# Optimization experiments

Measured on AMD Instinct MI355X. Metric: run time of the kernel, lower is better.

## Reference

```python
import jax, jax.numpy as jnp
import numpy as np

# Problem sizes (batched graph of G molecules)
N = 100_000   # total nodes
E = 400_000   # total directed edges
G = 2_500     # number of molecule graphs
K = 3         # len(idx_wo_smiles) -> zero rows inserted
NODE_F = 74   # graph_feats_shape[0]
EDGE_F = 12   # graph_feats_shape[1]
HID = 128     # hidden_feats = dim // 2
DIM = 256     # dim


def setup_inputs() -> dict:
    key = jax.random.key(0)
    ks = jax.random.split(key, 20)
    init = lambda k, shape, fan: (jax.random.normal(k, shape, jnp.float32) / np.sqrt(fan)).astype(jnp.float32)

    node_feats = jax.random.normal(ks[0], (N, NODE_F), jnp.float32)
    edge_feats = jax.random.normal(ks[1], (E, EDGE_F), jnp.float32)  # passed but unused by GCN
    src = jax.random.randint(ks[2], (E,), 0, N)
    dst = jax.random.randint(ks[3], (E,), 0, N)
    # sorted graph ids, every graph non-empty (~40 atoms each)
    graph_ids = (jnp.arange(N) * G) // N
    idx_wo_smiles = jnp.arange(K)

    return {
        'node_feats': node_feats,
        'edge_feats': edge_feats,
        'W1': init(ks[4], (NODE_F, HID), NODE_F), 'b1': jnp.zeros((HID,), jnp.float32),
        'Wr1': init(ks[5], (NODE_F, HID), NODE_F), 'br1': jnp.zeros((HID,), jnp.float32),
        'W2': init(ks[6], (HID, HID), HID), 'b2': jnp.zeros((HID,), jnp.float32),
        'Wr2': init(ks[7], (HID, HID), HID), 'br2': jnp.zeros((HID,), jnp.float32),
        'w_atom': init(ks[8], (HID, 1), HID), 'b_atom': jnp.zeros((1,), jnp.float32),
        'Wp1': init(ks[9], (2 * HID, HID), 2 * HID), 'bp1': jnp.zeros((HID,), jnp.float32),
        'Wp2': init(ks[10], (HID, DIM), HID), 'bp2': jnp.zeros((DIM,), jnp.float32),
        'src': src, 'dst': dst, 'graph_ids': graph_ids, 'idx_wo_smiles': idx_wo_smiles,
    }


def reference(node_feats, edge_feats, W1, b1, Wr1, br1, W2, b2, Wr2, br2,
              w_atom, b_atom, Wp1, bp1, Wp2, bp2, src, dst, graph_ids, idx_wo_smiles):
    n = node_feats.shape[0]
    ones_e = jnp.ones(src.shape[0], jnp.float32)
    out_deg = jax.ops.segment_sum(ones_e, src, num_segments=n)
    in_deg = jax.ops.segment_sum(ones_e, dst, num_segments=n)
    norm_s = jax.lax.rsqrt(jnp.maximum(out_deg, 1.0))  # [N]
    norm_d = jax.lax.rsqrt(jnp.maximum(in_deg, 1.0))   # [N]

    def gcn_layer(h, W, b, Wr, br):
        # GraphConv(norm='both'): D^-1/2 A D^-1/2 h W + b, with relu activation
        m = h[src] * norm_s[src][:, None]                       # [E, F] gather
        agg = jax.ops.segment_sum(m, dst, num_segments=n)       # [N, F] scatter-add
        gc = jax.nn.relu((agg * norm_d[:, None]) @ W + b)
        res = jax.nn.relu(h @ Wr + br)                          # residual connection
        return gc + res

    h = gcn_layer(node_feats, W1, b1, Wr1, br1)   # [N, HID]
    h = gcn_layer(h, W2, b2, Wr2, br2)            # [N, HID]

    # WeightedSumAndMax readout per molecule
    aw = jax.nn.sigmoid(h @ w_atom + b_atom)                          # [N, 1]
    hsum = jax.ops.segment_sum(h * aw, graph_ids, num_segments=G)     # [G, HID]
    hmax = jax.ops.segment_max(h, graph_ids, num_segments=G)          # [G, HID]
    gfeat = jnp.concatenate([hsum, hmax], axis=1)                     # [G, 2*HID]

    latent = jax.nn.relu(gfeat @ Wp1 + bp1) @ Wp2 + bp2               # [G, DIM]

    # Insert zero rows at idx_wo_smiles (sorted ascending -> final positions)
    total = G + idx_wo_smiles.shape[0]
    zero_mask = jnp.zeros((total,), bool).at[idx_wo_smiles].set(True)
    keep = jnp.nonzero(~zero_mask, size=G)[0]
    out = jnp.zeros((total, latent.shape[1]), latent.dtype).at[keep].set(latent)
    return out
```

## Files before the change

kernel.cpp:

```cpp
#include <hip/hip_runtime.h>
#include <hip/hip_bf16.h>
#include <stdint.h>

#define NODE_F 74
#define HID 128
#define DIM 256

typedef __hip_bfloat16 bf16;
typedef unsigned int u32;
typedef unsigned short u16;

typedef short s16x8 __attribute__((ext_vector_type(8)));
typedef __bf16 bf16x8 __attribute__((ext_vector_type(8)));
typedef float f32x4 __attribute__((ext_vector_type(4)));

__device__ __forceinline__ float rdl(float v, int l){
  return __int_as_float(__builtin_amdgcn_readlane(__float_as_int(v), l));
}
__device__ __forceinline__ float2 bfpair(u32 u){
  float2 r;
  r.x = __uint_as_float(u << 16);
  r.y = __uint_as_float(u & 0xffff0000u);
  return r;
}
__device__ __forceinline__ u32 packbf(float a, float b){
  u32 lo = (u32)__bfloat16_as_ushort(__float2bfloat16(a));
  u32 hi = (u32)__bfloat16_as_ushort(__float2bfloat16(b));
  return lo | (hi << 16);
}
__device__ __forceinline__ u16 bfbits(float a){
  return __bfloat16_as_ushort(__float2bfloat16(a));
}

__global__ void k_deg_prep(const int* __restrict__ src, const int* __restrict__ dst_,
                           float* __restrict__ outdeg_f, int* __restrict__ indeg, int E_,
                           const float* __restrict__ W1, const float* __restrict__ Wr1,
                           const float* __restrict__ W2, const float* __restrict__ Wr2,
                           u16* __restrict__ Bp1, u16* __restrict__ Bp2){
  int e = blockIdx.x*256 + threadIdx.x;
  if (e < E_){
    atomicAdd(&outdeg_f[src[e]], 1.0f);
    atomicAdd(&indeg[dst_[e]], 1);
  }
  int idx = e;
  if (idx < 57344){
    const float* W; u16* dstp; int S, Ktrue, loc;
    if      (idx < 12288){ W = W1;  dstp = Bp1;          S = 3; Ktrue = NODE_F; loc = idx; }
    else if (idx < 24576){ W = Wr1; dstp = Bp1 + 12288;  S = 3; Ktrue = NODE_F; loc = idx - 12288; }
    else if (idx < 40960){ W = W2;  dstp = Bp2;          S = 4; Ktrue = HID;    loc = idx - 24576; }
    else                 { W = Wr2; dstp = Bp2 + 16384;  S = 4; Ktrue = HID;    loc = idx - 40960; }
    const int el  = loc & 7;
    const int l   = (loc >> 3) & 63;
    const int rem = loc >> 9;
    const int s   = rem % S;
    const int t   = rem / S;
    const int k   = s*32 + (l >> 4)*8 + el;
    const int c   = t*16 + (l & 15);
    const float v = (k < Ktrue) ? W[(size_t)k*HID + c] : 0.f;
    dstp[loc] = bfbits(v);
  }
}

__global__ __launch_bounds__(256) void k_scan_a(const int* __restrict__ indeg,
                                                float* __restrict__ norm_s,
                                                float* __restrict__ norm_d,
                                                int* __restrict__ bsum, int n){
  __shared__ int red[256];
  const int base = blockIdx.x*1024 + threadIdx.x*4;
  int s = 0;
  #pragma unroll
  for (int i = 0; i < 4; ++i){
    const int idx = base + i;
    if (idx < n){
      const int d = indeg[idx];
      s += d;
      norm_d[idx] = rsqrtf(fmaxf((float)d, 1.0f));
      norm_s[idx] = rsqrtf(fmaxf(norm_s[idx], 1.0f));
    }
  }
  red[threadIdx.x] = s;
  __syncthreads();
  #pragma unroll
  for (int off = 128; off; off >>= 1){
    if (threadIdx.x < off) red[threadIdx.x] += red[threadIdx.x + off];
    __syncthreads();
  }
  if (threadIdx.x == 0) bsum[blockIdx.x] = red[0];
}

__global__ __launch_bounds__(1024) void k_scan_b(int* __restrict__ bsum, int nb){
  __shared__ int part[1024];
  __shared__ int carry;
  if (threadIdx.x == 0) carry = 0;
  __syncthreads();
  for (int c0 = 0; c0 < nb; c0 += 1024){
    const int tid = threadIdx.x, idx = c0 + tid;
    part[tid] = (idx < nb) ? bsum[idx] : 0;
    __syncthreads();
    for (int off = 1; off < 1024; off <<= 1){
      const int t = (tid >= off) ? part[tid-off] : 0;
      __syncthreads();
      part[tid] += t;
      __syncthreads();
    }
    if (idx < nb) bsum[idx] = carry + ((tid == 0) ? 0 : part[tid-1]);
    __syncthreads();
    if (tid == 0) carry += part[1023];
    __syncthreads();
  }
}

__global__ __launch_bounds__(256) void k_scan_c(int* __restrict__ indeg,
                                                const int* __restrict__ bsum,
                                                int* __restrict__ row_ptr, int n){
  __shared__ int part[256];
  const int base = blockIdx.x*1024 + threadIdx.x*4;
  int v[4]; int s = 0;
  #pragma unroll
  for (int i = 0; i < 4; ++i){
    const int idx = base + i;
    v[i] = (idx < n) ? indeg[idx] : 0;
    s += v[i];
  }
  part[threadIdx.x] = s;
  __syncthreads();
  for (int off = 1; off < 256; off <<= 1){
    const int t = (threadIdx.x >= off) ? part[threadIdx.x-off] : 0;
    __syncthreads();
    part[threadIdx.x] += t;
    __syncthreads();
  }
  int run = bsum[blockIdx.x] + ((threadIdx.x == 0) ? 0 : part[threadIdx.x-1]);
  #pragma unroll
  for (int i = 0; i < 4; ++i){
    const int idx = base + i;
    if (idx < n){
      row_ptr[idx] = run;
      run += v[i];
      indeg[idx] = 0;
    }
    if (idx == n-1) row_ptr[n] = run;
  }
}

__global__ void k_fill_conv(const int* __restrict__ src, const int* __restrict__ dst,
                            const int* __restrict__ row_ptr, int* __restrict__ cursor,
                            int* __restrict__ col, int E_,
                            const float* __restrict__ x0,
                            const float* __restrict__ norm_s,
                            u32* __restrict__ x0bf, int n, int do_conv){
  int e = blockIdx.x*256 + threadIdx.x;
  if (e < E_){
    int d = dst[e];
    int pos = row_ptr[d] + atomicAdd(&cursor[d], 1);
    col[pos] = src[e];
  }
  if (do_conv){
    const int tot = n*48;
    if (e < tot){
      const int r = e/48, l = e - r*48;
      const int f0 = 2*l, f1 = 2*l + 1;
      const float ns = norm_s[r];
      const float u0 = (f0 < NODE_F) ? ns*x0[(size_t)r*NODE_F + f0] : 0.f;
      const float u1 = (f1 < NODE_F) ? ns*x0[(size_t)r*NODE_F + f1] : 0.f;
      x0bf[e] = packbf(u0, u1);
    }
  }
}

__global__ __launch_bounds__(256, 8) void k_gather1b(
    const u32* __restrict__ x0bf, const int* __restrict__ row_ptr,
    const int* __restrict__ col, const float* __restrict__ norm_d,
    u32* __restrict__ ag1, int n){
  const int lane = threadIdx.x & 63;
  const int wv   = (blockIdx.x*256 + threadIdx.x) >> 6;
  const int r0   = wv*2;
  if (r0 >= n) return;
  int p[2], e[2];
  p[0] = row_ptr[r0]; e[0] = row_ptr[r0+1];
  const bool ok1 = (r0+1) < n;
  p[1] = ok1 ? e[0] : 0;
  e[1] = ok1 ? row_ptr[r0+2] : 0;
  const bool act = (lane < 48);
  const u32* xb = x0bf + lane;
  float a0[2] = {0.f,0.f}, a1[2] = {0.f,0.f};
  while ((p[0] < e[0]) | (p[1] < e[1])){
    int c[2], s[2][4];
    #pragma unroll
    for (int i = 0; i < 2; ++i){
      int d = e[i] - p[i];
      c[i] = (d > 4) ? 4 : ((d < 0) ? 0 : d);
      if (c[i] > 0){
        #pragma unroll
        for (int j = 0; j < 4; ++j)
          s[i][j] = col[p[i] + ((j < c[i]) ? j : (c[i]-1))];
      }
    }
    u32 v[2][4];
    #pragma unroll
    for (int i = 0; i < 2; ++i){
      #pragma unroll
      for (int j = 0; j < 4; ++j) v[i][j] = 0u;
      if (c[i] > 0 && act){
        #pragma unroll
        for (int j = 0; j < 4; ++j){
          const u32 t = xb[(size_t)s[i][j]*48];
          v[i][j] = (j < c[i]) ? t : 0u;
        }
      }
    }
    #pragma unroll
    for (int i = 0; i < 2; ++i){
      const float2 f0 = bfpair(v[i][0]), f1 = bfpair(v[i][1]);
      const float2 f2 = bfpair(v[i][2]), f3 = bfpair(v[i][3]);
      a0[i] += (f0.x + f1.x) + (f2.x + f3.x);
      a1[i] += (f0.y + f1.y) + (f2.y + f3.y);
      p[i] += c[i];
    }
  }
  if (lane < 48){
    #pragma unroll
    for (int i = 0; i < 2; ++i){
      const int row = r0 + i;
      if (row < n){
        const float nd = norm_d[row];
        ag1[(size_t)row*48 + lane] = packbf(a0[i]*nd, a1[i]*nd);
      }
    }
  }
}

__global__ __launch_bounds__(256, 8) void k_gather2b(
    const u32* __restrict__ h1u, const int* __restrict__ row_ptr,
    const int* __restrict__ col, const float* __restrict__ norm_s,
    const float* __restrict__ norm_d, u32* __restrict__ ag2, int n){
  const int lane = threadIdx.x & 63;
  const int wv   = (blockIdx.x*256 + threadIdx.x) >> 6;
  const int r0   = wv*2;
  if (r0 >= n) return;
  int p[2], e[2];
  p[0] = row_ptr[r0]; e[0] = row_ptr[r0+1];
  const bool ok1 = (r0+1) < n;
  p[1] = ok1 ? e[0] : 0;
  e[1] = ok1 ? row_ptr[r0+2] : 0;
  const u32* hb = h1u + lane;
  float a0[2] = {0.f,0.f}, a1[2] = {0.f,0.f};
  while ((p[0] < e[0]) | (p[1] < e[1])){
    int c[2], s[2][4];
    #pragma unroll
    for (int i = 0; i < 2; ++i){
      int d = e[i] - p[i];
      c[i] = (d > 4) ? 4 : ((d < 0) ? 0 : d);
      if (c[i] > 0){
        #pragma unroll
        for (int j = 0; j < 4; ++j)
          s[i][j] = col[p[i] + ((j < c[i]) ? j : (c[i]-1))];
      }
    }
    float nw[2][4];
    u32 v[2][4];
    #pragma unroll
    for (int i = 0; i < 2; ++i){
      #pragma unroll
      for (int j = 0; j < 4; ++j){ nw[i][j] = 0.f; v[i][j] = 0u; }
      if (c[i] > 0){
        #pragma unroll
        for (int j = 0; j < 4; ++j) nw[i][j] = (j < c[i]) ? norm_s[s[i][j]] : 0.f;
        #pragma unroll
        for (int j = 0; j < 4; ++j) v[i][j] = hb[(size_t)s[i][j]*64];
      }
    }
    #pragma unroll
    for (int i = 0; i < 2; ++i){
      const float2 f0 = bfpair(v[i][0]), f1 = bfpair(v[i][1]);
      const float2 f2 = bfpair(v[i][2]), f3 = bfpair(v[i][3]);
      a0[i] = fmaf(f0.x, nw[i][0], fmaf(f1.x, nw[i][1],
              fmaf(f2.x, nw[i][2], fmaf(f3.x, nw[i][3], a0[i]))));
      a1[i] = fmaf(f0.y, nw[i][0], fmaf(f1.y, nw[i][1],
              fmaf(f2.y, nw[i][2], fmaf(f3.y, nw[i][3], a1[i]))));
      p[i] += c[i];
    }
  }
  #pragma unroll
  for (int i = 0; i < 2; ++i){
    const int row = r0 + i;
    if (row < n){
      const float nd = norm_d[row];
      ag2[(size_t)row*64 + lane] = packbf(a0[i]*nd, a1[i]*nd);
    }
  }
}

__global__ __launch_bounds__(256) void k_gather1f(
    const float* __restrict__ x0, const int* __restrict__ row_ptr,
    const int* __restrict__ col, const float* __restrict__ norm_s,
    const float* __restrict__ norm_d, u32* __restrict__ ag1, int n){
  const int lane = threadIdx.x & 63;
  const int row  = blockIdx.x*4 + (threadIdx.x >> 6);
  if (row >= n) return;
  const int p0 = row_ptr[row], p1 = row_ptr[row+1];
  const bool act = (lane < 37);
  const float* xb = x0 + 2*lane;
  float a0 = 0.f, a1 = 0.f;
  int p = p0;
  #pragma unroll 1
  for (; p + 3 < p1; p += 4){
    const int s0 = col[p], s1 = col[p+1], s2 = col[p+2], s3 = col[p+3];
    const float n0 = norm_s[s0], n1 = norm_s[s1], n2 = norm_s[s2], n3 = norm_s[s3];
    float2 v0{0.f,0.f}, v1{0.f,0.f}, v2{0.f,0.f}, v3{0.f,0.f};
    if (act){
      v0 = *(const float2*)&xb[(size_t)s0*NODE_F];
      v1 = *(const float2*)&xb[(size_t)s1*NODE_F];
      v2 = *(const float2*)&xb[(size_t)s2*NODE_F];
      v3 = *(const float2*)&xb[(size_t)s3*NODE_F];
    }
    a0 = fmaf(v0.x,n0, fmaf(v1.x,n1, fmaf(v2.x,n2, fmaf(v3.x,n3, a0))));
    a1 = fmaf(v0.y,n0, fmaf(v1.y,n1, fmaf(v2.y,n2, fmaf(v3.y,n3, a1))));
  }
  const int rem = p1 - p;
  if (rem > 0){
    const int s0 = col[p];
    int s1 = s0, s2 = s0;
    float n1 = 0.f, n2 = 0.f;
    const float n0 = norm_s[s0];
    if (rem > 1){ s1 = col[p+1]; n1 = norm_s[s1]; }
    if (rem > 2){ s2 = col[p+2]; n2 = norm_s[s2]; }
    float2 v0{0.f,0.f}, v1{0.f,0.f}, v2{0.f,0.f};
    if (act){
      v0 = *(const float2*)&xb[(size_t)s0*NODE_F];
      v1 = *(const float2*)&xb[(size_t)s1*NODE_F];
      v2 = *(const float2*)&xb[(size_t)s2*NODE_F];
    }
    a0 = fmaf(v0.x,n0, fmaf(v1.x,n1, fmaf(v2.x,n2, a0)));
    a1 = fmaf(v0.y,n0, fmaf(v1.y,n1, fmaf(v2.y,n2, a1)));
  }
  if (lane < 48){
    const float nd = norm_d[row];
    ag1[(size_t)row*48 + lane] = packbf(a0*nd, a1*nd);
  }
}

__global__ __launch_bounds__(256) void k_gather2f(
    const u32* __restrict__ h1u, const int* __restrict__ row_ptr,
    const int* __restrict__ col, const float* __restrict__ norm_s,
    const float* __restrict__ norm_d, u32* __restrict__ ag2, int n){
  const int lane = threadIdx.x & 63;
  const int row  = blockIdx.x*4 + (threadIdx.x >> 6);
  if (row >= n) return;
  const int p0 = row_ptr[row], p1 = row_ptr[row+1];
  const u32* hb = h1u + lane;
  float a0 = 0.f, a1 = 0.f;
  int p = p0;
  #pragma unroll 1
  for (; p + 3 < p1; p += 4){
    const int s0 = col[p], s1 = col[p+1], s2 = col[p+2], s3 = col[p+3];
    const float n0 = norm_s[s0], n1 = norm_s[s1], n2 = norm_s[s2], n3 = norm_s[s3];
    const u32 u0 = hb[(size_t)s0*64];
    const u32 u1 = hb[(size_t)s1*64];
    const u32 u2 = hb[(size_t)s2*64];
    const u32 u3 = hb[(size_t)s3*64];
    const float2 f0 = bfpair(u0), f1 = bfpair(u1), f2 = bfpair(u2), f3 = bfpair(u3);
    a0 = fmaf(f0.x,n0, fmaf(f1.x,n1, fmaf(f2.x,n2, fmaf(f3.x,n3, a0))));
    a1 = fmaf(f0.y,n0, fmaf(f1.y,n1, fmaf(f2.y,n2, fmaf(f3.y,n3, a1))));
  }
  const int rem = p1 - p;
  if (rem > 0){
    const int s0 = col[p];
    int s1 = s0, s2 = s0;
    float n1 = 0.f, n2 = 0.f;
    const float n0 = norm_s[s0];
    if (rem > 1){ s1 = col[p+1]; n1 = norm_s[s1]; }
    if (rem > 2){ s2 = col[p+2]; n2 = norm_s[s2]; }
    const u32 u0 = hb[(size_t)s0*64];
    const u32 u1 = hb[(size_t)s1*64];
    const u32 u2 = hb[(size_t)s2*64];
    const float2 f0 = bfpair(u0), f1 = bfpair(u1), f2 = bfpair(u2);
    a0 = fmaf(f0.x,n0, fmaf(f1.x,n1, fmaf(f2.x,n2, a0)));
    a1 = fmaf(f0.y,n0, fmaf(f1.y,n1, fmaf(f2.y,n2, a1)));
  }
  const float nd = norm_d[row];
  ag2[(size_t)row*64 + lane] = packbf(a0*nd, a1*nd);
}

__global__ __launch_bounds__(256) void k_ggemm1(
    const u16* __restrict__ ag1, const float* __restrict__ x0,
    const u16* __restrict__ Bp, const float* __restrict__ bg_,
    const float* __restrict__ br_, u16* __restrict__ h1, int n){
  constexpr int FR1 = 8*3*512;
  __shared__ __align__(16) u16 sB[2*FR1];
  {
    const uint4* s4 = (const uint4*)Bp;
    uint4* d4 = (uint4*)sB;
    #pragma unroll
    for (int i = 0; i < 12; ++i)
      d4[threadIdx.x + i*256] = s4[threadIdx.x + i*256];
  }
  __syncthreads();
  const int lane = threadIdx.x & 63;
  const int wid  = threadIdx.x >> 6;
  const int jg = lane & 15, kg = lane >> 4;
  const int kb = kg*8;
  const int nb = (n + 63) >> 6;
  for (int bt = blockIdx.x; bt < nb; bt += gridDim.x){
    const int r0 = bt*64 + wid*16;
    if (r0 >= n) continue;
    const int row = r0 + jg;
    const bool rok = row < n;
    const int rA = rok ? row : (n-1);

    bf16x8 ag[3], ar[3];
    #pragma unroll
    for (int s = 0; s < 3; ++s)
      ag[s] = __builtin_bit_cast(bf16x8, *(const s16x8*)&ag1[(size_t)rA*96 + s*32 + kb]);
    {
      const float* px = x0 + (size_t)rA*NODE_F;
      #pragma unroll
      for (int s = 0; s < 2; ++s)
        #pragma unroll
        for (int e = 0; e < 8; e += 2){
          const float2 w = *(const float2*)&px[s*32 + kb + e];
          ar[s][e]   = (__bf16)w.x;
          ar[s][e+1] = (__bf16)w.y;
        }
      #pragma unroll
      for (int e = 0; e < 8; ++e) ar[2][e] = (__bf16)0.f;
      if (kg == 0){
        #pragma unroll
        for (int e = 0; e < 8; e += 2){
          const float2 w = *(const float2*)&px[64 + e];
          ar[2][e]   = (__bf16)w.x;
          ar[2][e+1] = (__bf16)w.y;
        }
      } else if (kg == 1){
        const float2 w = *(const float2*)&px[72];
        ar[2][0] = (__bf16)w.x;
        ar[2][1] = (__bf16)w.y;
      }
    }

    f32x4 accg[8], accr[8];
    #pragma unroll
    for (int t = 0; t < 8; ++t){
      accg[t] = f32x4{0.f,0.f,0.f,0.f};
      accr[t] = f32x4{0.f,0.f,0.f,0.f};
    }
    #pragma unroll
    for (int s = 0; s < 3; ++s){
      #pragma unroll
      for (int t = 0; t < 8; ++t){
        const bf16x8 bg = __builtin_bit_cast(bf16x8,
            *(const s16x8*)&sB[((t*3 + s)*64 + lane)*8]);
        const bf16x8 br = __builtin_bit_cast(bf16x8,
            *(const s16x8*)&sB[FR1 + ((t*3 + s)*64 + lane)*8]);
        accg[t] = __builtin_amdgcn_mfma_f32_16x16x32_bf16(ag[s], bg, accg[t], 0,0,0);
        accr[t] = __builtin_amdgcn_mfma_f32_16x16x32_bf16(ar[s], br, accr[t], 0,0,0);
      }
    }

    const int rowb = r0 + 4*kg;
    #pragma unroll
    for (int t = 0; t < 8; ++t){
      const int colc = t*16 + jg;
      const float bgv = bg_[colc], brv = br_[colc];
      #pragma unroll
      for (int r = 0; r < 4; ++r){
        const int row2 = rowb + r;
        if (row2 < n){
          const float o = fmaxf(accg[t][r] + bgv, 0.f) + fmaxf(accr[t][r] + brv, 0.f);
          h1[(size_t)row2*HID + colc] = bfbits(o);
        }
      }
    }
  }
}

__global__ __launch_bounds__(256) void k_ggemm2(
    const u16* __restrict__ ag2, const u16* __restrict__ h1,
    const u16* __restrict__ Bp, const float* __restrict__ bg_,
    const float* __restrict__ br_,
    const float* __restrict__ w_atom, const float* __restrict__ b_atom,
    const int* __restrict__ gid,
    float* __restrict__ hsum, u32* __restrict__ hmax, int n){
  constexpr int FR2 = 8*4*512;
  __shared__ __align__(16) u16 sB[2*FR2];
  {
    const uint4* s4 = (const uint4*)Bp;
    uint4* d4 = (uint4*)sB;
    #pragma unroll
    for (int i = 0; i < 16; ++i)
      d4[threadIdx.x + i*256] = s4[threadIdx.x + i*256];
  }
  __syncthreads();
  const int lane = threadIdx.x & 63;
  const int wid  = threadIdx.x >> 6;
  const int jg = lane & 15, kg = lane >> 4;
  const int kb = kg*8;
  const int nb = (n + 63) >> 6;
  for (int bt = blockIdx.x; bt < nb; bt += gridDim.x){
    const int r0 = bt*64 + wid*16;
    if (r0 >= n) continue;
    const int row = r0 + jg;
    const bool rok = row < n;
    const int rA = rok ? row : (n-1);

    f32x4 accg[8], accr[8];
    #pragma unroll
    for (int t = 0; t < 8; ++t){
      accg[t] = f32x4{0.f,0.f,0.f,0.f};
      accr[t] = f32x4{0.f,0.f,0.f,0.f};
    }
    #pragma unroll
    for (int s = 0; s < 4; ++s){
      const bf16x8 agf = __builtin_bit_cast(bf16x8,
          *(const s16x8*)&ag2[(size_t)rA*HID + s*32 + kb]);
      const bf16x8 arf = __builtin_bit_cast(bf16x8,
          *(const s16x8*)&h1[(size_t)rA*HID + s*32 + kb]);
      #pragma unroll
      for (int t = 0; t < 8; ++t){
        const bf16x8 bg = __builtin_bit_cast(bf16x8,
            *(const s16x8*)&sB[((t*4 + s)*64 + lane)*8]);
        const bf16x8 br = __builtin_bit_cast(bf16x8,
            *(const s16x8*)&sB[FR2 + ((t*4 + s)*64 + lane)*8]);
        accg[t] = __builtin_amdgcn_mfma_f32_16x16x32_bf16(agf, bg, accg[t], 0,0,0);
        accr[t] = __builtin_amdgcn_mfma_f32_16x16x32_bf16(arf, br, accr[t], 0,0,0);
      }
    }

    float o[8][4];
    #pragma unroll
    for (int t = 0; t < 8; ++t){
      const int colc = t*16 + jg;
      const float bgv = bg_[colc], brv = br_[colc];
      #pragma unroll
      for (int r = 0; r < 4; ++r)
        o[t][r] = fmaxf(accg[t][r] + bgv, 0.f) + fmaxf(accr[t][r] + brv, 0.f);
    }
    float wa[8];
    #pragma unroll
    for (int t = 0; t < 8; ++t) wa[t] = w_atom[t*16 + jg];
    const float ba = b_atom[0];
    const int rowb = r0 + 4*kg;
    float awv[4]; int gidr[4];
    #pragma unroll
    for (int r = 0; r < 4; ++r){
      const int row2 = rowb + r;
      float dot = 0.f;
      #pragma unroll
      for (int t = 0; t < 8; ++t) dot = fmaf(o[t][r], wa[t], dot);
      dot += __shfl_xor(dot, 1);
      dot += __shfl_xor(dot, 2);
      dot += __shfl_xor(dot, 4);
      dot += __shfl_xor(dot, 8);
      awv[r]  = 1.0f/(1.0f + __expf(-(dot + ba)));
      gidr[r] = (row2 < n) ? gid[row2] : -1;
    }
    const int rhi    = (r0 + 15 < n) ? (r0 + 15) : (n - 1);
    const int gfirst = gid[r0];
    const int glast  = gid[rhi];
    for (int g = gfirst; g <= glast; ++g){
      #pragma unroll
      for (int t = 0; t < 8; ++t){
        float sv = 0.f, mv = 0.f;
        #pragma unroll
        for (int r = 0; r < 4; ++r){
          const bool in = (gidr[r] == g);
          sv += in ? o[t][r]*awv[r] : 0.f;
          mv  = in ? fmaxf(mv, o[t][r]) : mv;
        }
        sv += __shfl_xor(sv, 16);
        sv += __shfl_xor(sv, 32);
        mv  = fmaxf(mv, __shfl_xor(mv, 16));
        mv  = fmaxf(mv, __shfl_xor(mv, 32));
        if (lane < 16){
          atomicAdd(&hsum[(size_t)g*HID + t*16 + jg], sv);
          atomicMax(&hmax[(size_t)g*HID + t*16 + jg], __float_as_uint(mv));
        }
      }
    }
  }
}

__global__ __launch_bounds__(256) void k_mlp(
    const float* __restrict__ hsum, const float* __restrict__ hmaxf,
    const float* __restrict__ Wp1, const float* __restrict__ bp1,
    const float* __restrict__ Wp2, const float* __restrict__ bp2,
    const int* __restrict__ idxw, int K_,
    float* __restrict__ out, int G_){
  const int lane = threadIdx.x & 63;
  const int row = blockIdx.x*4 + (threadIdx.x >> 6);
  if (blockIdx.x == 0){
    for (int j = 0; j < K_; ++j){
      const int zr = idxw[j];
      for (int i = threadIdx.x; i < DIM; i += 256)
        out[(size_t)zr*DIM + i] = 0.f;
    }
  }
  if (row >= G_) return;
  const int c = lane*2;
  float ra0 = hsum [(size_t)row*HID + lane];
  float ra1 = hsum [(size_t)row*HID + 64 + lane];
  float ra2 = hmaxf[(size_t)row*HID + lane];
  float ra3 = hmaxf[(size_t)row*HID + 64 + lane];
  float a0 = 0.f, a1 = 0.f;
  #pragma unroll 4
  for (int k = 0; k < 64; ++k){
    const float v0 = rdl(ra0,k), v1 = rdl(ra1,k), v2 = rdl(ra2,k), v3 = rdl(ra3,k);
    const float2 w0 = *(const float2*)&Wp1[(size_t)(k      )*HID + c];
    const float2 w1 = *(const float2*)&Wp1[(size_t)(k +  64)*HID + c];
    const float2 w2 = *(const float2*)&Wp1[(size_t)(k + 128)*HID + c];
    const float2 w3 = *(const float2*)&Wp1[(size_t)(k + 192)*HID + c];
    a0 = fmaf(v0,w0.x, fmaf(v1,w1.x, fmaf(v2,w2.x, fmaf(v3,w3.x, a0))));
    a1 = fmaf(v0,w0.y, fmaf(v1,w1.y, fmaf(v2,w2.y, fmaf(v3,w3.y, a1))));
  }
  const float h0  = fmaxf(a0 + bp1[c],   0.f);
  const float h1v = fmaxf(a1 + bp1[c+1], 0.f);
  const int c4 = lane*4;
  float acc0=0.f, acc1=0.f, acc2=0.f, acc3=0.f;
  #pragma unroll 4
  for (int j = 0; j < 64; ++j){
    const float he = rdl(h0, j);
    const float ho = rdl(h1v, j);
    const float4 we = *(const float4*)&Wp2[(size_t)(2*j  )*DIM + c4];
    const float4 wo = *(const float4*)&Wp2[(size_t)(2*j+1)*DIM + c4];
    acc0 = fmaf(he,we.x, fmaf(ho,wo.x, acc0));
    acc1 = fmaf(he,we.y, fmaf(ho,wo.y, acc1));
    acc2 = fmaf(he,we.z, fmaf(ho,wo.z, acc2));
    acc3 = fmaf(he,we.w, fmaf(ho,wo.w, acc3));
  }
  int orow = row;
  for (int j = 0; j < K_; ++j){ if (idxw[j] <= orow) orow++; }
  float* po = out + (size_t)orow*DIM + c4;
  po[0] = acc0 + bp2[c4];
  po[1] = acc1 + bp2[c4+1];
  po[2] = acc2 + bp2[c4+2];
  po[3] = acc3 + bp2[c4+3];
}

extern "C" void kernel_launch(void* const* d_in, const int* in_sizes, int n_in,
                              void* d_out, int out_size, void* d_ws, size_t ws_size,
                              hipStream_t stream){
  (void)n_in;
  const float* x0     = (const float*)d_in[0];
  const float* W1     = (const float*)d_in[2];
  const float* b1     = (const float*)d_in[3];
  const float* Wr1    = (const float*)d_in[4];
  const float* br1    = (const float*)d_in[5];
  const float* W2     = (const float*)d_in[6];
  const float* b2     = (const float*)d_in[7];
  const float* Wr2    = (const float*)d_in[8];
  const float* br2    = (const float*)d_in[9];
  const float* w_atom = (const float*)d_in[10];
  const float* b_atom = (const float*)d_in[11];
  const float* Wp1    = (const float*)d_in[12];
  const float* bp1    = (const float*)d_in[13];
  const float* Wp2    = (const float*)d_in[14];
  const float* bp2    = (const float*)d_in[15];
  const int* src  = (const int*)d_in[16];
  const int* dst  = (const int*)d_in[17];
  const int* gid  = (const int*)d_in[18];
  const int* idxw = (const int*)d_in[19];

  const int N_ = in_sizes[0] / NODE_F;
  const int E_ = in_sizes[16];
  const int K_ = in_sizes[19];
  const int G_ = out_size / DIM - K_;

  u16*   h1     = (u16*)d_ws;
  float* norm_d = (float*)(h1 + (size_t)N_*HID);
  float* norm_s = norm_d + N_;
  float* hsum   = norm_s + N_;
  float* hmaxv  = hsum + (size_t)G_*HID;
  int*   indeg  = (int*)(hmaxv + (size_t)G_*HID);
  int*   row_ptr= indeg + N_;
  int*   col    = row_ptr + ((N_ + 4) & ~3);
  int*   bsum   = col + ((E_ + 4) & ~3);
  const int nscan = (N_ + 1023)/1024;
  uintptr_t aggp = ((uintptr_t)(bsum + nscan) + 255) & ~(uintptr_t)255;
  u32* aggu = (u32*)aggp;
  uintptr_t x0bfp = aggp + (size_t)N_*64*sizeof(u32);
  u32* x0bf = (u32*)x0bfp;
  const size_t need_bf = (x0bfp + (size_t)N_*48*sizeof(u32)) - (uintptr_t)d_ws;
  const bool use_bf = (ws_size >= need_bf);

  u16*   Bp1    = (u16*)d_out;
  u16*   Bp2    = Bp1 + 2*12288;

  hipMemsetAsync(norm_s, 0, ((size_t)2*N_ + (size_t)2*G_*HID)*sizeof(float), stream);

  k_deg_prep<<<(E_+255)/256, 256, 0, stream>>>(src, dst, norm_s, indeg, E_,
                                               W1, Wr1, W2, Wr2, Bp1, Bp2);
  k_scan_a  <<<nscan, 256, 0, stream>>>(indeg, norm_s, norm_d, bsum, N_);
  k_scan_b  <<<1, 1024, 0, stream>>>(bsum, nscan);
  k_scan_c  <<<nscan, 256, 0, stream>>>(indeg, bsum, row_ptr, N_);

  const int conv_tot = use_bf ? (N_*48 > E_ ? N_*48 : E_) : E_;
  k_fill_conv<<<(conv_tot+255)/256, 256, 0, stream>>>(
      src, dst, row_ptr, indeg, col, E_, x0, norm_s,
      use_bf ? x0bf : aggu, N_, use_bf ? 1 : 0);

  const int nb   = (N_ + 63) / 64;
  const int nbw  = (N_ + 3) / 4;
  const int nbw2 = (N_ + 7) / 8;
  const int g1   = (nb < 768) ? nb : 768;
  const int g2   = (nb < 512) ? nb : 512;
  if (use_bf){
    k_gather1b<<<nbw2, 256, 0, stream>>>(x0bf, row_ptr, col, norm_d, aggu, N_);
  } else {
    k_gather1f<<<nbw, 256, 0, stream>>>(x0, row_ptr, col, norm_s, norm_d, aggu, N_);
  }
  k_ggemm1<<<g1, 256, 0, stream>>>((const u16*)aggu, x0, Bp1, b1, br1, h1, N_);
  if (use_bf){
    k_gather2b<<<nbw2, 256, 0, stream>>>((const u32*)h1, row_ptr, col, norm_s,
                                         norm_d, aggu, N_);
  } else {
    k_gather2f<<<nbw, 256, 0, stream>>>((const u32*)h1, row_ptr, col, norm_s,
                                        norm_d, aggu, N_);
  }
  k_ggemm2<<<g2, 256, 0, stream>>>((const u16*)aggu, h1, Bp2, b2, br2,
                                   w_atom, b_atom, gid, hsum, (u32*)hmaxv, N_);

  k_mlp<<<(G_+3)/4, 256, 0, stream>>>(hsum, hmaxv, Wp1, bp1, Wp2, bp2,
                                      idxw, K_, (float*)d_out, G_);
}
```

Measured before the change: 337.8 us.

## Pre-scale h1 by norm_s in GEMM1 epilogue and widen GEMM blocks to 512 threads

The layer-1 GEMM epilogue now also writes a second bf16 copy of h1 already multiplied by the per-row source norm. A new gather kernel (k_gather2s) then sums neighbour rows without loading norm_s per edge, which removes the per-edge dependent norm lookups. Both GEMM kernels move to 512-thread blocks that cover 128 rows each, so the shared-memory weight staging is amortised over more rows, and the fp32 fallback gather2f is dropped. The cost is an extra N×128 bf16 write and more workspace, and the pre-scaled path only runs when the workspace is large enough.

```diff
diff --git a/kernel.cpp b/kernel.cpp
--- a/kernel.cpp
+++ b/kernel.cpp
@@ -226,6 +226,65 @@
         const float nd = norm_d[row];
         ag1[(size_t)row*48 + lane] = packbf(a0[i]*nd, a1[i]*nd);
       }
+    }
+  }
+}
+
+__global__ __launch_bounds__(256, 8) void k_gather2s(
+    const u32* __restrict__ h1su, const int* __restrict__ row_ptr,
+    const int* __restrict__ col, const float* __restrict__ norm_d,
+    u32* __restrict__ ag2, int n){
+  const int lane = threadIdx.x & 63;
+  const int wv   = (blockIdx.x*256 + threadIdx.x) >> 6;
+  const int r0   = wv*2;
+  if (r0 >= n) return;
+  int p[2], e[2];
+  p[0] = row_ptr[r0]; e[0] = row_ptr[r0+1];
+  const bool ok1 = (r0+1) < n;
+  p[1] = ok1 ? e[0] : 0;
+  e[1] = ok1 ? row_ptr[r0+2] : 0;
+  const u32* hb = h1su + lane;
+  float a0[2] = {0.f,0.f}, a1[2] = {0.f,0.f};
+  while ((p[0] < e[0]) | (p[1] < e[1])){
+    int c[2], s[2][4];
+    #pragma unroll
+    for (int i = 0; i < 2; ++i){
+      int d = e[i] - p[i];
+      c[i] = (d > 4) ? 4 : ((d < 0) ? 0 : d);
+      if (c[i] > 0){
+        #pragma unroll
+        for (int j = 0; j < 4; ++j)
+          s[i][j] = col[p[i] + ((j < c[i]) ? j : (c[i]-1))];
+      }
+    }
+    u32 v[2][4];
+    #pragma unroll
+    for (int i = 0; i < 2; ++i){
+      #pragma unroll
+      for (int j = 0; j < 4; ++j) v[i][j] = 0u;
+      if (c[i] > 0){
+        #pragma unroll
+        for (int j = 0; j < 4; ++j){
+          const u32 t = hb[(size_t)s[i][j]*64];
+          v[i][j] = (j < c[i]) ? t : 0u;
+        }
+      }
+    }
+    #pragma unroll
+    for (int i = 0; i < 2; ++i){
+      const float2 f0 = bfpair(v[i][0]), f1 = bfpair(v[i][1]);
+      const float2 f2 = bfpair(v[i][2]), f3 = bfpair(v[i][3]);
+      a0[i] += (f0.x + f1.x) + (f2.x + f3.x);
+      a1[i] += (f0.y + f1.y) + (f2.y + f3.y);
+      p[i] += c[i];
+    }
+  }
+  #pragma unroll
+  for (int i = 0; i < 2; ++i){
+    const int row = r0 + i;
+    if (row < n){
+      const float nd = norm_d[row];
+      ag2[(size_t)row*64 + lane] = packbf(a0[i]*nd, a1[i]*nd);
     }
   }
 }
@@ -340,69 +399,28 @@
   }
 }
 
-__global__ __launch_bounds__(256) void k_gather2f(
-    const u32* __restrict__ h1u, const int* __restrict__ row_ptr,
-    const int* __restrict__ col, const float* __restrict__ norm_s,
-    const float* __restrict__ norm_d, u32* __restrict__ ag2, int n){
-  const int lane = threadIdx.x & 63;
-  const int row  = blockIdx.x*4 + (threadIdx.x >> 6);
-  if (row >= n) return;
-  const int p0 = row_ptr[row], p1 = row_ptr[row+1];
-  const u32* hb = h1u + lane;
-  float a0 = 0.f, a1 = 0.f;
-  int p = p0;
-  #pragma unroll 1
-  for (; p + 3 < p1; p += 4){
-    const int s0 = col[p], s1 = col[p+1], s2 = col[p+2], s3 = col[p+3];
-    const float n0 = norm_s[s0], n1 = norm_s[s1], n2 = norm_s[s2], n3 = norm_s[s3];
-    const u32 u0 = hb[(size_t)s0*64];
-    const u32 u1 = hb[(size_t)s1*64];
-    const u32 u2 = hb[(size_t)s2*64];
-    const u32 u3 = hb[(size_t)s3*64];
-    const float2 f0 = bfpair(u0), f1 = bfpair(u1), f2 = bfpair(u2), f3 = bfpair(u3);
-    a0 = fmaf(f0.x,n0, fmaf(f1.x,n1, fmaf(f2.x,n2, fmaf(f3.x,n3, a0))));
-    a1 = fmaf(f0.y,n0, fmaf(f1.y,n1, fmaf(f2.y,n2, fmaf(f3.y,n3, a1))));
-  }
-  const int rem = p1 - p;
-  if (rem > 0){
-    const int s0 = col[p];
-    int s1 = s0, s2 = s0;
-    float n1 = 0.f, n2 = 0.f;
-    const float n0 = norm_s[s0];
-    if (rem > 1){ s1 = col[p+1]; n1 = norm_s[s1]; }
-    if (rem > 2){ s2 = col[p+2]; n2 = norm_s[s2]; }
-    const u32 u0 = hb[(size_t)s0*64];
-    const u32 u1 = hb[(size_t)s1*64];
-    const u32 u2 = hb[(size_t)s2*64];
-    const float2 f0 = bfpair(u0), f1 = bfpair(u1), f2 = bfpair(u2);
-    a0 = fmaf(f0.x,n0, fmaf(f1.x,n1, fmaf(f2.x,n2, a0)));
-    a1 = fmaf(f0.y,n0, fmaf(f1.y,n1, fmaf(f2.y,n2, a1)));
-  }
-  const float nd = norm_d[row];
-  ag2[(size_t)row*64 + lane] = packbf(a0*nd, a1*nd);
-}
-
-__global__ __launch_bounds__(256) void k_ggemm1(
+__global__ __launch_bounds__(512) void k_ggemm1(
     const u16* __restrict__ ag1, const float* __restrict__ x0,
     const u16* __restrict__ Bp, const float* __restrict__ bg_,
-    const float* __restrict__ br_, u16* __restrict__ h1, int n){
+    const float* __restrict__ br_, const float* __restrict__ norm_s,
+    u16* __restrict__ h1, u16* __restrict__ h1s, int wh1s, int n){
   constexpr int FR1 = 8*3*512;
   __shared__ __align__(16) u16 sB[2*FR1];
   {
     const uint4* s4 = (const uint4*)Bp;
     uint4* d4 = (uint4*)sB;
     #pragma unroll
-    for (int i = 0; i < 12; ++i)
-      d4[threadIdx.x + i*256] = s4[threadIdx.x + i*256];
+    for (int i = 0; i < 6; ++i)
+      d4[threadIdx.x + i*512] = s4[threadIdx.x + i*512];
   }
   __syncthreads();
   const int lane = threadIdx.x & 63;
   const int wid  = threadIdx.x >> 6;
   const int jg = lane & 15, kg = lane >> 4;
   const int kb = kg*8;
-  const int nb = (n + 63) >> 6;
+  const int nb = (n + 127) >> 7;
   for (int bt = blockIdx.x; bt < nb; bt += gridDim.x){
-    const int r0 = bt*64 + wid*16;
+    const int r0 = bt*128 + wid*16;
     if (r0 >= n) continue;
     const int row = r0 + jg;
     const bool rok = row < n;
@@ -458,6 +476,10 @@
     }
 
     const int rowb = r0 + 4*kg;
+    float ns4[4];
+    #pragma unroll
+    for (int r = 0; r < 4; ++r)
+      ns4[r] = (wh1s && rowb + r < n) ? norm_s[rowb + r] : 0.f;
     #pragma unroll
     for (int t = 0; t < 8; ++t){
       const int colc = t*16 + jg;
@@ -468,13 +490,14 @@
         if (row2 < n){
           const float o = fmaxf(accg[t][r] + bgv, 0.f) + fmaxf(accr[t][r] + brv, 0.f);
           h1[(size_t)row2*HID + colc] = bfbits(o);
+          if (wh1s) h1s[(size_t)row2*HID + colc] = bfbits(o * ns4[r]);
         }
       }
     }
   }
 }
 
-__global__ __launch_bounds__(256) void k_ggemm2(
+__global__ __launch_bounds__(512) void k_ggemm2(
     const u16* __restrict__ ag2, const u16* __restrict__ h1,
     const u16* __restrict__ Bp, const float* __restrict__ bg_,
     const float* __restrict__ br_,
@@ -487,17 +510,17 @@
     const uint4* s4 = (const uint4*)Bp;
     uint4* d4 = (uint4*)sB;
     #pragma unroll
-    for (int i = 0; i < 16; ++i)
-      d4[threadIdx.x + i*256] = s4[threadIdx.x + i*256];
+    for (int i = 0; i < 8; ++i)
+      d4[threadIdx.x + i*512] = s4[threadIdx.x + i*512];
   }
   __syncthreads();
   const int lane = threadIdx.x & 63;
   const int wid  = threadIdx.x >> 6;
   const int jg = lane & 15, kg = lane >> 4;
   const int kb = kg*8;
-  const int nb = (n + 63) >> 6;
+  const int nb = (n + 127) >> 7;
   for (int bt = blockIdx.x; bt < nb; bt += gridDim.x){
-    const int r0 = bt*64 + wid*16;
+    const int r0 = bt*128 + wid*16;
     if (r0 >= n) continue;
     const int row = r0 + jg;
     const bool rok = row < n;
@@ -681,6 +704,10 @@
   u32* x0bf = (u32*)x0bfp;
   const size_t need_bf = (x0bfp + (size_t)N_*48*sizeof(u32)) - (uintptr_t)d_ws;
   const bool use_bf = (ws_size >= need_bf);
+  uintptr_t h1sp = x0bfp + (size_t)N_*48*sizeof(u32);
+  u16* h1s = (u16*)h1sp;
+  const size_t need_h1s = (h1sp + (size_t)N_*HID*sizeof(u16)) - (uintptr_t)d_ws;
+  const bool use_h1s = use_bf && (ws_size >= need_h1s);
 
   u16*   Bp1    = (u16*)d_out;
   u16*   Bp2    = Bp1 + 2*12288;
@@ -698,25 +725,25 @@
       src, dst, row_ptr, indeg, col, E_, x0, norm_s,
       use_bf ? x0bf : aggu, N_, use_bf ? 1 : 0);
 
-  const int nb   = (N_ + 63) / 64;
   const int nbw  = (N_ + 3) / 4;
   const int nbw2 = (N_ + 7) / 8;
-  const int g1   = (nb < 768) ? nb : 768;
-  const int g2   = (nb < 512) ? nb : 512;
+  const int nb7  = (N_ + 127) / 128;
+  const int gg   = (nb7 < 512) ? nb7 : 512;
   if (use_bf){
     k_gather1b<<<nbw2, 256, 0, stream>>>(x0bf, row_ptr, col, norm_d, aggu, N_);
   } else {
     k_gather1f<<<nbw, 256, 0, stream>>>(x0, row_ptr, col, norm_s, norm_d, aggu, N_);
   }
-  k_ggemm1<<<g1, 256, 0, stream>>>((const u16*)aggu, x0, Bp1, b1, br1, h1, N_);
-  if (use_bf){
+  k_ggemm1<<<gg, 512, 0, stream>>>((const u16*)aggu, x0, Bp1, b1, br1, norm_s,
+                                   h1, h1s, use_h1s ? 1 : 0, N_);
+  if (use_h1s){
+    k_gather2s<<<nbw2, 256, 0, stream>>>((const u32*)h1s, row_ptr, col, norm_d,
+                                         aggu, N_);
+  } else {
     k_gather2b<<<nbw2, 256, 0, stream>>>((const u32*)h1, row_ptr, col, norm_s,
                                          norm_d, aggu, N_);
-  } else {
-    k_gather2f<<<nbw, 256, 0, stream>>>((const u32*)h1, row_ptr, col, norm_s,
-                                        norm_d, aggu, N_);
-  }
-  k_ggemm2<<<g2, 256, 0, stream>>>((const u16*)aggu, h1, Bp2, b2, br2,
+  }
+  k_ggemm2<<<gg, 512, 0, stream>>>((const u16*)aggu, h1, Bp2, b2, br2,
                                    w_atom, b_atom, gid, hsum, (u32*)hmaxv, N_);
 
   k_mlp<<<(G_+3)/4, 256, 0, stream>>>(hsum, hmaxv, Wp1, bp1, Wp2, bp2,
```

After: 335.1 us. Within noise of the previous version (-0.8%).
